# Kernel optimization log

Hardware: AMD Instinct MI355X
Metric: run time of the kernel (lower is better)

## Reference

```python
import jax, jax.numpy as jnp
import numpy as np

N, B, D = 2048, 4, 2048   # seq_len, batch, embed_dim (sequence-first layout)
E = 2                     # expand_ratio
H = D // E                # number of heads
EPS = 1e-5


def setup_inputs() -> dict:
    key = jax.random.key(0)
    ks = jax.random.split(key, 3)
    x = jax.random.normal(ks[0], (N, B, D), dtype=jnp.float32)
    W_in = jax.random.normal(ks[1], (3 * D, D), dtype=jnp.float32) / np.sqrt(D).astype(np.float32)
    b_in = jnp.zeros((3 * D,), jnp.float32)
    W_out = jax.random.normal(ks[2], (D, D), dtype=jnp.float32) / np.sqrt(D).astype(np.float32)
    b_out = jnp.zeros((D,), jnp.float32)
    gamma = jnp.ones((D,), jnp.float32)
    beta = jnp.zeros((D,), jnp.float32)
    return {"x": x, "W_in": W_in, "b_in": b_in, "gamma": gamma, "beta": beta,
            "W_out": W_out, "b_out": b_out}


def _linear_scan(lam, u):
    # h_t = lam_t * h_{t-1} + u_t along time axis 0 (HgruRealFunction)
    def combine(c1, c2):
        a1, b1 = c1
        a2, b2 = c2
        return a1 * a2, a2 * b1 + b2
    _, h = jax.lax.associative_scan(combine, (lam, u), axis=0)
    return h


def _layernorm(x, gamma, beta):
    mu = jnp.mean(x, axis=-1, keepdims=True)
    var = jnp.var(x, axis=-1, keepdims=True)
    return (x - mu) * jax.lax.rsqrt(var + EPS) * gamma + beta


def reference(x, W_in, b_in, gamma, beta, W_out, b_out):
    n, b, d = x.shape
    feat = x @ W_in.T + b_in                       # (n,b,3d)
    inp, og, fg = jnp.split(feat, 3, axis=-1)
    inp = jax.nn.silu(inp)                         # act_fun = silu
    og = jax.nn.sigmoid(og)                        # uv_act_fun = sigmoid
    lam = jax.nn.sigmoid(fg)                       # lower_bound = 0 => lambda = sigmoid(F)

    inp = inp.reshape(n, b, H, E)
    og = og.reshape(n, b, H, E)
    lam = lam.reshape(n, b, H, E)

    # input = einsum('...hd,...he->...hde', 1-lambda, input)
    u = ((1.0 - lam)[..., :, None] * inp[..., None, :]).reshape(n, b, H * E * E)
    lam_f = jnp.broadcast_to(lam[..., :, None], (n, b, H, E, E)).reshape(n, b, H * E * E)

    s_fwd = _linear_scan(lam_f, u)
    s_rev = jnp.flip(_linear_scan(jnp.flip(lam_f, 0), jnp.flip(u, 0)), 0)
    s = (s_fwd + s_rev).reshape(n, b, H, E, E)

    o = jnp.einsum('nbhde,nbhd->nbhe', s, og).reshape(n, b, d)
    o = _layernorm(o, gamma, beta)
    return o @ W_out.T + b_out
```

## Files before the change

### kernel.cpp

```cpp
#include <hip/hip_runtime.h>
#include <hip/hip_bf16.h>

#define NSEQ 2048
#define NB   4
#define DIM  2048
#define HN   1024
#define FC   6144
#define MROWS 8192
#define CHUNKS 64
#define CLEN 32
#define NCH  4096

typedef __bf16 bf16x8_t __attribute__((ext_vector_type(8)));
typedef float  f32x4_t  __attribute__((ext_vector_type(4)));

__device__ __forceinline__ float sigm(float x){ return 1.f/(1.f + __expf(-x)); }
__device__ __forceinline__ float bflo(unsigned p){ return __uint_as_float(p << 16); }
__device__ __forceinline__ float bfhi(unsigned p){ return __uint_as_float(p & 0xffff0000u); }
__device__ __forceinline__ unsigned short f2bf(float f){
  union { __hip_bfloat16 h; unsigned short u; } cv;
  cv.h = __float2bfloat16(f);
  return cv.u;
}

__global__ __launch_bounds__(256) void cvt_bf16_4(const float4* __restrict__ in,
                                                  ushort4* __restrict__ out, int n4){
  int i = blockIdx.x * blockDim.x + threadIdx.x;
  int st = gridDim.x * blockDim.x;
  for (; i < n4; i += st){
    float4 v = in[i];
    ushort4 r;
    r.x = f2bf(v.x); r.y = f2bf(v.y); r.z = f2bf(v.z); r.w = f2bf(v.w);
    out[i] = r;
  }
}

__device__ __forceinline__ void gl_lds16(const void* g, void* l){
  __builtin_amdgcn_global_load_lds((const __attribute__((address_space(1))) void*)g,
                                   (__attribute__((address_space(3))) void*)l, 16, 0, 0);
}

template <typename OutT>
__global__ __launch_bounds__(512, 2) void gemm256(const __hip_bfloat16* __restrict__ A,
                                                  const __hip_bfloat16* __restrict__ B,
                                                  const float* __restrict__ bias,
                                                  OutT* __restrict__ C,
                                                  int M, int N, int K, int nbx){
  __shared__ __align__(16) __hip_bfloat16 smem[3*16384];
  const int tid  = threadIdx.x;
  const int wave = tid >> 6, lane = tid & 63;

  const int cpx = gridDim.x >> 3;
  const int wg  = (blockIdx.x & 7) * cpx + (blockIdx.x >> 3);
  const int bx = wg % nbx, by = wg / nbx;
  const int m0 = by * 256, n0 = bx * 256;

  const int wr = wave >> 2, wc = wave & 3;
  const int r  = lane & 15, q = lane >> 4;
  const int kph = (q ^ (r & 3)) * 8;

  auto stage = [&](int kt, int bo){
    #pragma unroll
    for (int i = 0; i < 2; ++i){
      int g = i*512 + tid;
      int row = g >> 2;
      int k16 = (g & 3) ^ (row & 3);
      gl_lds16(A + (size_t)(m0 + row)*K + kt + k16*8, smem + bo + g*8);
      gl_lds16(B + (size_t)(n0 + row)*K + kt + k16*8, smem + bo + 8192 + g*8);
    }
  };
  const int arow = (wr*128 + r) * 32 + kph;
  const int brow = 8192 + (wc*64 + r) * 32 + kph;

  f32x4_t acc[8][4] = {};
  const int NT = K >> 5;

  stage(0, 0);
  stage(32, 16384);
  __syncthreads();

  bf16x8_t Fa[8], Fb[4];
  #pragma unroll
  for (int i = 0; i < 8; ++i) Fa[i] = *reinterpret_cast<const bf16x8_t*>(smem + arow + i*512);
  #pragma unroll
  for (int j = 0; j < 4; ++j) Fb[j] = *reinterpret_cast<const bf16x8_t*>(smem + brow + j*512);

  for (int t = 0; t < NT; ++t){
    int b2 = 16384 * ((t+2) % 3);
    if (t + 2 < NT) stage((t+2)*32, b2);
    int rb = (t+1 < NT) ? 16384*((t+1)%3) : 16384*(t%3);
    bf16x8_t Na[8], Nb[4];
    #pragma unroll
    for (int j = 0; j < 4; ++j) Nb[j] = *reinterpret_cast<const bf16x8_t*>(smem + rb + brow + j*512);
    #pragma unroll
    for (int i = 0; i < 8; ++i) Na[i] = *reinterpret_cast<const bf16x8_t*>(smem + rb + arow + i*512);
    __builtin_amdgcn_s_setprio(1);
    #pragma unroll
    for (int i = 0; i < 8; ++i)
      #pragma unroll
      for (int j = 0; j < 4; ++j)
        acc[i][j] = __builtin_amdgcn_mfma_f32_16x16x32_bf16(Fa[i], Fb[j], acc[i][j], 0, 0, 0);
    __builtin_amdgcn_s_setprio(0);
    __syncthreads();
    #pragma unroll
    for (int i = 0; i < 8; ++i) Fa[i] = Na[i];
    #pragma unroll
    for (int j = 0; j < 4; ++j) Fb[j] = Nb[j];
  }

  #pragma unroll
  for (int fn = 0; fn < 4; ++fn){
    int col = n0 + wc*64 + fn*16 + r;
    float bv = bias[col];
    #pragma unroll
    for (int fm = 0; fm < 8; ++fm){
      int row0 = m0 + wr*128 + fm*16 + q*4;
      #pragma unroll
      for (int j = 0; j < 4; ++j){
        float v = acc[fm][fn][j] + bv;
        if constexpr (__is_same(OutT, float))
          C[(size_t)(row0 + j)*N + col] = v;
        else
          C[(size_t)(row0 + j)*N + col] = __float2bfloat16(v);
      }
    }
  }
}

struct SV { float l0, l1, u00, u01, u10, u11; };
__device__ __forceinline__ SV stepv(const unsigned* __restrict__ fp, int rowu){
  unsigned pi = fp[rowu];
  unsigned pf = fp[rowu + 2048];
  SV s;
  s.l0 = sigm(bflo(pf)); s.l1 = sigm(bfhi(pf));
  float i0 = bflo(pi), i1 = bfhi(pi);
  i0 *= sigm(i0); i1 *= sigm(i1);
  float a0 = 1.f - s.l0, a1 = 1.f - s.l1;
  s.u00 = a0*i0; s.u01 = a0*i1; s.u10 = a1*i0; s.u11 = a1*i1;
  return s;
}

__global__ __launch_bounds__(256) void scan_agg(const unsigned* __restrict__ feat,
    float* __restrict__ aggP, float4* __restrict__ aggHF, float4* __restrict__ aggHR){
  int ch = blockIdx.x*256 + threadIdx.x;
  int c  = blockIdx.y;
  int b = ch >> 10, h = ch & 1023;
  int base = b*3072 + h;
  int n0 = c*CLEN;
  float P0 = 1.f, P1 = 1.f;
  float f00=0,f01=0,f10=0,f11=0;
  for (int t = 0; t < CLEN; ++t){
    SV s = stepv(feat, (n0+t)*12288 + base);
    f00 = s.l0*f00 + s.u00; f01 = s.l0*f01 + s.u01;
    f10 = s.l1*f10 + s.u10; f11 = s.l1*f11 + s.u11;
    P0 *= s.l0; P1 *= s.l1;
  }
  float r00=0,r01=0,r10=0,r11=0;
  for (int t = CLEN-1; t >= 0; --t){
    SV s = stepv(feat, (n0+t)*12288 + base);
    r00 = s.l0*r00 + s.u00; r01 = s.l0*r01 + s.u01;
    r10 = s.l1*r10 + s.u10; r11 = s.l1*r11 + s.u11;
  }
  aggP[c*8192 + ch*2]     = P0;
  aggP[c*8192 + ch*2 + 1] = P1;
  aggHF[c*4096 + ch] = make_float4(f00,f01,f10,f11);
  aggHR[c*4096 + ch] = make_float4(r00,r01,r10,r11);
}

__global__ __launch_bounds__(256) void scan_carry(const float* __restrict__ aggP,
    const float* __restrict__ aggHF, const float* __restrict__ aggHR,
    float* __restrict__ cF, float* __restrict__ cR){
  int t  = blockIdx.x*256 + threadIdx.x;
  int pd = t >> 1;
  float s = 0.f;
  for (int c = 0; c < CHUNKS; ++c){
    cF[c*16384 + t] = s;
    s = aggP[c*8192 + pd]*s + aggHF[c*16384 + t];
  }
  s = 0.f;
  for (int c = CHUNKS-1; c >= 0; --c){
    cR[c*16384 + t] = s;
    s = aggP[c*8192 + pd]*s + aggHR[c*16384 + t];
  }
}

__global__ __launch_bounds__(256) void scan_fr(const unsigned* __restrict__ feat,
    const float4* __restrict__ cF, const float4* __restrict__ cR,
    float2* __restrict__ o){
  int ch = blockIdx.x*256 + threadIdx.x;
  int c  = blockIdx.y;
  int b = ch >> 10, h = ch & 1023;
  int base = b*3072 + h;
  float2 accv[CLEN];
  {
    float4 hv = cF[c*4096 + ch];
    float h00=hv.x, h01=hv.y, h10=hv.z, h11=hv.w;
    #pragma unroll
    for (int t = 0; t < CLEN; ++t){
      int rowu = (c*CLEN + t)*12288 + base;
      SV s = stepv(feat, rowu);
      h00 = s.l0*h00 + s.u00; h01 = s.l0*h01 + s.u01;
      h10 = s.l1*h10 + s.u10; h11 = s.l1*h11 + s.u11;
      unsigned po = feat[rowu + 1024];
      float g0 = sigm(bflo(po)), g1 = sigm(bfhi(po));
      accv[t] = make_float2(g0*h00 + g1*h10, g0*h01 + g1*h11);
    }
  }
  {
    float4 hv = cR[c*4096 + ch];
    float h00=hv.x, h01=hv.y, h10=hv.z, h11=hv.w;
    #pragma unroll
    for (int t = CLEN-1; t >= 0; --t){
      int rowu = (c*CLEN + t)*12288 + base;
      SV s = stepv(feat, rowu);
      h00 = s.l0*h00 + s.u00; h01 = s.l0*h01 + s.u01;
      h10 = s.l1*h10 + s.u10; h11 = s.l1*h11 + s.u11;
      unsigned po = feat[rowu + 1024];
      float g0 = sigm(bflo(po)), g1 = sigm(bfhi(po));
      accv[t].x += g0*h00 + g1*h10;
      accv[t].y += g0*h01 + g1*h11;
    }
  }
  #pragma unroll
  for (int t = 0; t < CLEN; ++t)
    o[((c*CLEN + t)*NB + b)*1024 + h] = accv[t];
}

__global__ __launch_bounds__(256) void layernorm_k(const float* __restrict__ o,
    const float* __restrict__ gamma, const float* __restrict__ beta,
    __hip_bfloat16* __restrict__ out){
  int row = blockIdx.x, t = threadIdx.x;
  const float4* x = (const float4*)(o + (size_t)row*DIM);
  float4 a = x[t], b = x[t + 256];
  float s  = (a.x + a.y) + (a.z + a.w) + (b.x + b.y) + (b.z + b.w);
  float ss = (a.x*a.x + a.y*a.y) + (a.z*a.z + a.w*a.w)
           + (b.x*b.x + b.y*b.y) + (b.z*b.z + b.w*b.w);
  #pragma unroll
  for (int off = 32; off > 0; off >>= 1){
    s  += __shfl_down(s, off);
    ss += __shfl_down(ss, off);
  }
  __shared__ float red[8];
  int wv = t >> 6, ln = t & 63;
  if (ln == 0){ red[wv] = s; red[4 + wv] = ss; }
  __syncthreads();
  float S  = (red[0] + red[1]) + (red[2] + red[3]);
  float SS = (red[4] + red[5]) + (red[6] + red[7]);
  float mu = S * (1.f/DIM);
  float rs = rsqrtf(SS * (1.f/DIM) - mu*mu + 1e-5f);
  const float4* gp = (const float4*)gamma;
  const float4* bp = (const float4*)beta;
  float4 g0 = gp[t], g1 = gp[t + 256], be0 = bp[t], be1 = bp[t + 256];
  ushort4* op = (ushort4*)(out + (size_t)row*DIM);
  ushort4 r0, r1;
  r0.x = f2bf((a.x - mu)*rs*g0.x + be0.x);
  r0.y = f2bf((a.y - mu)*rs*g0.y + be0.y);
  r0.z = f2bf((a.z - mu)*rs*g0.z + be0.z);
  r0.w = f2bf((a.w - mu)*rs*g0.w + be0.w);
  r1.x = f2bf((b.x - mu)*rs*g1.x + be1.x);
  r1.y = f2bf((b.y - mu)*rs*g1.y + be1.y);
  r1.z = f2bf((b.z - mu)*rs*g1.z + be1.z);
  r1.w = f2bf((b.w - mu)*rs*g1.w + be1.w);
  op[t] = r0; op[t + 256] = r1;
}

extern "C" void kernel_launch(void* const* d_in, const int* in_sizes, int n_in,
                              void* d_out, int out_size, void* d_ws, size_t ws_size,
                              hipStream_t stream){
  (void)in_sizes; (void)n_in; (void)out_size;
  const float* x     = (const float*)d_in[0];
  const float* W_in  = (const float*)d_in[1];
  const float* b_in  = (const float*)d_in[2];
  const float* gamma = (const float*)d_in[3];
  const float* beta  = (const float*)d_in[4];
  const float* W_out = (const float*)d_in[5];
  const float* b_out = (const float*)d_in[6];
  float* out = (float*)d_out;

  char* p = (char*)d_ws;
  auto carve = [&](size_t bytes) -> char* {
    char* r = p; p += (bytes + 255) & ~(size_t)255; return r;
  };
  __hip_bfloat16* feat = (__hip_bfloat16*)carve((size_t)MROWS*FC*2);
  char* U              = carve((size_t)MROWS*DIM*4);
  __hip_bfloat16* Wob  = (__hip_bfloat16*)carve((size_t)DIM*DIM*2);
  float* aggP  = (float*)carve((size_t)CHUNKS*8192*4);
  float* aggHF = (float*)carve((size_t)CHUNKS*16384*4);
  float* aggHR = (float*)carve((size_t)CHUNKS*16384*4);
  float* cF    = (float*)carve((size_t)CHUNKS*16384*4);
  float* cR    = (float*)carve((size_t)CHUNKS*16384*4);
  if ((size_t)(p - (char*)d_ws) > ws_size) return;

  __hip_bfloat16* xb  = (__hip_bfloat16*)U;
  __hip_bfloat16* Wib = (__hip_bfloat16*)(U + (size_t)MROWS*DIM*2);
  float* o            = (float*)U;
  __hip_bfloat16* oln = (__hip_bfloat16*)feat;

  cvt_bf16_4<<<2048, 256, 0, stream>>>((const float4*)x,     (ushort4*)xb,  MROWS*DIM/4);
  cvt_bf16_4<<<2048, 256, 0, stream>>>((const float4*)W_in,  (ushort4*)Wib, FC*DIM/4);
  cvt_bf16_4<<<1024, 256, 0, stream>>>((const float4*)W_out, (ushort4*)Wob, DIM*DIM/4);

  gemm256<__hip_bfloat16><<<768, 512, 0, stream>>>(xb, Wib, b_in, feat, MROWS, FC, 2048, FC/256);

  scan_agg  <<<dim3(NCH/256, CHUNKS), 256, 0, stream>>>((const unsigned*)feat, aggP, (float4*)aggHF, (float4*)aggHR);
  scan_carry<<<64, 256, 0, stream>>>(aggP, aggHF, aggHR, cF, cR);
  scan_fr   <<<dim3(NCH/256, CHUNKS), 256, 0, stream>>>((const unsigned*)feat, (const float4*)cF, (const float4*)cR, (float2*)o);

  layernorm_k<<<MROWS, 256, 0, stream>>>(o, gamma, beta, oln);

  gemm256<float><<<256, 512, 0, stream>>>(oln, Wob, b_out, out, MROWS, DIM, 2048, DIM/256);
}
```

Measured before the change: 496.5 us.

## Restructure GEMM main loop into 8-phase ping-pong pipeline with half-tile staging

Rewrites the bf16 GEMM main loop to use a K tile of 64 split into half-tiles across two LDS slots (128KB of LDS). Each of eight phases loads fragments, issues one half-tile global-to-LDS load, then synchronizes with explicit vmcnt/lgkmcnt waits and raw barriers before a block of MFMAs. It also switches to a new XOR swizzle layout with two rows packed per 64-element line. The aim is finer-grained overlap of memory and MFMA work with fewer full syncthreads. In exchange, the LDS use doubles, which with launch_bounds(512,2) may limit occupancy, and the hand-tuned waitcnt counts are fragile.

```diff
diff --git a/kernel.cpp b/kernel.cpp
--- a/kernel.cpp
+++ b/kernel.cpp
@@ -40,13 +40,42 @@
                                    (__attribute__((address_space(3))) void*)l, 16, 0, 0);
 }
 
+template<int SLOT,int KSUB,int MH,bool VM, class SG>
+__device__ __forceinline__ void do_phase(const __hip_bfloat16* smem,
+    const int* aoff, const int* boff, bf16x8_t (&Bf)[4], f32x4_t (&acc)[8][4], SG&& sg){
+  if (VM) asm volatile("s_waitcnt vmcnt(6)" ::: "memory");
+  const __hip_bfloat16* base = smem + SLOT*32768 + KSUB*8192;
+  bf16x8_t Af[4];
+  #pragma unroll
+  for (int mi = 0; mi < 4; ++mi)
+    Af[mi] = *reinterpret_cast<const bf16x8_t*>(base + aoff[MH*4 + mi]);
+  if (MH == 0){
+    #pragma unroll
+    for (int n = 0; n < 4; ++n)
+      Bf[n] = *reinterpret_cast<const bf16x8_t*>(base + 16384 + boff[n]);
+  }
+  sg();
+  __builtin_amdgcn_s_barrier();
+  asm volatile("s_waitcnt lgkmcnt(0)" ::: "memory");
+  __builtin_amdgcn_sched_barrier(0);
+  __builtin_amdgcn_s_setprio(1);
+  #pragma unroll
+  for (int mi = 0; mi < 4; ++mi)
+    #pragma unroll
+    for (int n = 0; n < 4; ++n)
+      acc[MH*4 + mi][n] =
+        __builtin_amdgcn_mfma_f32_16x16x32_bf16(Af[mi], Bf[n], acc[MH*4 + mi][n], 0, 0, 0);
+  __builtin_amdgcn_s_setprio(0);
+  __builtin_amdgcn_s_barrier();
+}
+
 template <typename OutT>
 __global__ __launch_bounds__(512, 2) void gemm256(const __hip_bfloat16* __restrict__ A,
                                                   const __hip_bfloat16* __restrict__ B,
                                                   const float* __restrict__ bias,
                                                   OutT* __restrict__ C,
                                                   int M, int N, int K, int nbx){
-  __shared__ __align__(16) __hip_bfloat16 smem[3*16384];
+  __shared__ __align__(16) __hip_bfloat16 smem[65536];
   const int tid  = threadIdx.x;
   const int wave = tid >> 6, lane = tid & 63;
 
@@ -57,55 +86,55 @@
 
   const int wr = wave >> 2, wc = wave & 3;
   const int r  = lane & 15, q = lane >> 4;
-  const int kph = (q ^ (r & 3)) * 8;
-
-  auto stage = [&](int kt, int bo){
+  const int NT = K >> 6;
+
+  int aoff[8], boff[4];
+  #pragma unroll
+  for (int f = 0; f < 8; ++f){
+    int R = wr*128 + (f>>2)*64 + (f&3)*16 + r;
+    aoff[f] = (R>>1)*64 + (((((R&1)<<2) | q) ^ ((R>>1)&7)) << 3);
+  }
+  #pragma unroll
+  for (int n = 0; n < 4; ++n){
+    int R = wc*64 + n*16 + r;
+    boff[n] = (R>>1)*64 + (((((R&1)<<2) | q) ^ ((R>>1)&7)) << 3);
+  }
+
+  auto stage_half = [&](int slot, int ab, int khalf, int ktile){
+    if (ktile >= NT) return;
+    const __hip_bfloat16* Base = ab ? B : A;
+    const int t0 = ab ? n0 : m0;
+    const int kc = ktile*64 + khalf*32;
+    const int hb = slot*32768 + ab*16384 + khalf*8192;
     #pragma unroll
     for (int i = 0; i < 2; ++i){
       int g = i*512 + tid;
-      int row = g >> 2;
-      int k16 = (g & 3) ^ (row & 3);
-      gl_lds16(A + (size_t)(m0 + row)*K + kt + k16*8, smem + bo + g*8);
-      gl_lds16(B + (size_t)(n0 + row)*K + kt + k16*8, smem + bo + 8192 + g*8);
+      int line = g >> 3, glp = g & 7;
+      int glog = glp ^ (line & 7);
+      int row = line*2 + (glog >> 2);
+      int kg = glog & 3;
+      gl_lds16(Base + (size_t)(t0 + row)*K + kc + kg*8, smem + hb + g*8);
     }
   };
-  const int arow = (wr*128 + r) * 32 + kph;
-  const int brow = 8192 + (wc*64 + r) * 32 + kph;
 
   f32x4_t acc[8][4] = {};
-  const int NT = K >> 5;
-
-  stage(0, 0);
-  stage(32, 16384);
-  __syncthreads();
-
-  bf16x8_t Fa[8], Fb[4];
-  #pragma unroll
-  for (int i = 0; i < 8; ++i) Fa[i] = *reinterpret_cast<const bf16x8_t*>(smem + arow + i*512);
-  #pragma unroll
-  for (int j = 0; j < 4; ++j) Fb[j] = *reinterpret_cast<const bf16x8_t*>(smem + brow + j*512);
-
-  for (int t = 0; t < NT; ++t){
-    int b2 = 16384 * ((t+2) % 3);
-    if (t + 2 < NT) stage((t+2)*32, b2);
-    int rb = (t+1 < NT) ? 16384*((t+1)%3) : 16384*(t%3);
-    bf16x8_t Na[8], Nb[4];
-    #pragma unroll
-    for (int j = 0; j < 4; ++j) Nb[j] = *reinterpret_cast<const bf16x8_t*>(smem + rb + brow + j*512);
-    #pragma unroll
-    for (int i = 0; i < 8; ++i) Na[i] = *reinterpret_cast<const bf16x8_t*>(smem + rb + arow + i*512);
-    __builtin_amdgcn_s_setprio(1);
-    #pragma unroll
-    for (int i = 0; i < 8; ++i)
-      #pragma unroll
-      for (int j = 0; j < 4; ++j)
-        acc[i][j] = __builtin_amdgcn_mfma_f32_16x16x32_bf16(Fa[i], Fb[j], acc[i][j], 0, 0, 0);
-    __builtin_amdgcn_s_setprio(0);
-    __syncthreads();
-    #pragma unroll
-    for (int i = 0; i < 8; ++i) Fa[i] = Na[i];
-    #pragma unroll
-    for (int j = 0; j < 4; ++j) Fb[j] = Nb[j];
+  bf16x8_t Bf[4];
+
+  stage_half(0,0,0, 0); stage_half(0,1,0, 0); stage_half(0,0,1, 0); stage_half(0,1,1, 0);
+  stage_half(1,1,0, 1); stage_half(1,0,0, 1); stage_half(1,1,1, 1);
+  asm volatile("s_waitcnt vmcnt(6)" ::: "memory");
+  __builtin_amdgcn_s_barrier();
+
+  for (int j = 0; j < NT/2; ++j){
+    const int kb = 2*j;
+    do_phase<0,0,0,true >(smem, aoff, boff, Bf, acc, [&]{ stage_half(1,0,1, kb+1); });
+    do_phase<0,0,1,false>(smem, aoff, boff, Bf, acc, [&]{ stage_half(0,1,0, kb+2); });
+    do_phase<0,1,0,true >(smem, aoff, boff, Bf, acc, [&]{ stage_half(0,0,0, kb+2); });
+    do_phase<0,1,1,false>(smem, aoff, boff, Bf, acc, [&]{ stage_half(0,1,1, kb+2); });
+    do_phase<1,0,0,true >(smem, aoff, boff, Bf, acc, [&]{ stage_half(0,0,1, kb+2); });
+    do_phase<1,0,1,false>(smem, aoff, boff, Bf, acc, [&]{ stage_half(1,1,0, kb+3); });
+    do_phase<1,1,0,true >(smem, aoff, boff, Bf, acc, [&]{ stage_half(1,0,0, kb+3); });
+    do_phase<1,1,1,false>(smem, aoff, boff, Bf, acc, [&]{ stage_half(1,1,1, kb+3); });
   }
 
   #pragma unroll
@@ -116,12 +145,12 @@
     for (int fm = 0; fm < 8; ++fm){
       int row0 = m0 + wr*128 + fm*16 + q*4;
       #pragma unroll
-      for (int j = 0; j < 4; ++j){
-        float v = acc[fm][fn][j] + bv;
+      for (int jj = 0; jj < 4; ++jj){
+        float v = acc[fm][fn][jj] + bv;
         if constexpr (__is_same(OutT, float))
-          C[(size_t)(row0 + j)*N + col] = v;
+          C[(size_t)(row0 + jj)*N + col] = v;
         else
-          C[(size_t)(row0 + j)*N + col] = __float2bfloat16(v);
+          C[(size_t)(row0 + jj)*N + col] = __float2bfloat16(v);
       }
     }
   }
```

Measured after the change: 479.8 us. 3.4% less time.

## Switch GEMMs to 256x128 tiles with double buffering; cache scan inputs in registers

Applied to the files above, without the earlier changes.

Both GEMMs now use a 256x128 block tile with 256 threads (4 waves) instead of 256x256 with 512 threads. The LDS pipeline drops from triple to double buffering and gets a new XOR swizzle over row pairs. Register prefetch of the next fragments is replaced by loading fragments at the start of each iteration. The chunk-aggregate scan keeps its 32 loaded feature words per channel in registers, so the reverse pass does not reload them from global memory. Risks: less load/compute overlap in the GEMM, twice as many blocks, and higher register pressure in the scan kernel.

```diff
diff --git a/kernel.cpp b/kernel.cpp
--- a/kernel.cpp
+++ b/kernel.cpp
@@ -41,71 +41,79 @@
 }
 
 template <typename OutT>
-__global__ __launch_bounds__(512, 2) void gemm256(const __hip_bfloat16* __restrict__ A,
-                                                  const __hip_bfloat16* __restrict__ B,
-                                                  const float* __restrict__ bias,
-                                                  OutT* __restrict__ C,
-                                                  int M, int N, int K, int nbx){
-  __shared__ __align__(16) __hip_bfloat16 smem[3*16384];
+__global__ __launch_bounds__(256, 2) void gemm256x128(const __hip_bfloat16* __restrict__ A,
+                                                      const __hip_bfloat16* __restrict__ B,
+                                                      const float* __restrict__ bias,
+                                                      OutT* __restrict__ C,
+                                                      int M, int N, int K, int nbx){
+  __shared__ __align__(16) __hip_bfloat16 smem[2*12288];
   const int tid  = threadIdx.x;
   const int wave = tid >> 6, lane = tid & 63;
 
   const int cpx = gridDim.x >> 3;
   const int wg  = (blockIdx.x & 7) * cpx + (blockIdx.x >> 3);
   const int bx = wg % nbx, by = wg / nbx;
-  const int m0 = by * 256, n0 = bx * 256;
-
-  const int wr = wave >> 2, wc = wave & 3;
+  const int m0 = by * 256, n0 = bx * 128;
+
+  const int wr = wave >> 1, wc = wave & 1;
   const int r  = lane & 15, q = lane >> 4;
-  const int kph = (q ^ (r & 3)) * 8;
+  const int NT = K >> 5;
+
+  int aoff[8], boff[4];
+  #pragma unroll
+  for (int f = 0; f < 8; ++f){
+    int R = wr*128 + f*16 + r;
+    aoff[f] = (R>>1)*64 + (((((R&1)<<2) | q) ^ ((R>>1)&7)) << 3);
+  }
+  #pragma unroll
+  for (int n = 0; n < 4; ++n){
+    int R = wc*64 + n*16 + r;
+    boff[n] = (R>>1)*64 + (((((R&1)<<2) | q) ^ ((R>>1)&7)) << 3);
+  }
 
   auto stage = [&](int kt, int bo){
     #pragma unroll
+    for (int i = 0; i < 4; ++i){
+      int g = i*256 + tid;
+      int line = g >> 3, glog = (g & 7) ^ (line & 7);
+      int row = line*2 + (glog >> 2), kg = glog & 3;
+      gl_lds16(A + (size_t)(m0 + row)*K + kt + kg*8, smem + bo + g*8);
+    }
+    #pragma unroll
     for (int i = 0; i < 2; ++i){
-      int g = i*512 + tid;
-      int row = g >> 2;
-      int k16 = (g & 3) ^ (row & 3);
-      gl_lds16(A + (size_t)(m0 + row)*K + kt + k16*8, smem + bo + g*8);
-      gl_lds16(B + (size_t)(n0 + row)*K + kt + k16*8, smem + bo + 8192 + g*8);
+      int g = i*256 + tid;
+      int line = g >> 3, glog = (g & 7) ^ (line & 7);
+      int row = line*2 + (glog >> 2), kg = glog & 3;
+      gl_lds16(B + (size_t)(n0 + row)*K + kt + kg*8, smem + bo + 8192 + g*8);
     }
   };
-  const int arow = (wr*128 + r) * 32 + kph;
-  const int brow = 8192 + (wc*64 + r) * 32 + kph;
 
   f32x4_t acc[8][4] = {};
-  const int NT = K >> 5;
 
   stage(0, 0);
-  stage(32, 16384);
   __syncthreads();
-
-  bf16x8_t Fa[8], Fb[4];
-  #pragma unroll
-  for (int i = 0; i < 8; ++i) Fa[i] = *reinterpret_cast<const bf16x8_t*>(smem + arow + i*512);
-  #pragma unroll
-  for (int j = 0; j < 4; ++j) Fb[j] = *reinterpret_cast<const bf16x8_t*>(smem + brow + j*512);
+  int buf = 0;
 
   for (int t = 0; t < NT; ++t){
-    int b2 = 16384 * ((t+2) % 3);
-    if (t + 2 < NT) stage((t+2)*32, b2);
-    int rb = (t+1 < NT) ? 16384*((t+1)%3) : 16384*(t%3);
-    bf16x8_t Na[8], Nb[4];
-    #pragma unroll
-    for (int j = 0; j < 4; ++j) Nb[j] = *reinterpret_cast<const bf16x8_t*>(smem + rb + brow + j*512);
-    #pragma unroll
-    for (int i = 0; i < 8; ++i) Na[i] = *reinterpret_cast<const bf16x8_t*>(smem + rb + arow + i*512);
+    if (t + 1 < NT) stage((t+1)*32, (buf^1)*12288);
+    const __hip_bfloat16* Ab = smem + buf*12288;
+    const __hip_bfloat16* Bb = Ab + 8192;
+    bf16x8_t bfr[4], af[8];
+    #pragma unroll
+    for (int fn = 0; fn < 4; ++fn)
+      bfr[fn] = *reinterpret_cast<const bf16x8_t*>(Bb + boff[fn]);
+    #pragma unroll
+    for (int fm = 0; fm < 8; ++fm)
+      af[fm] = *reinterpret_cast<const bf16x8_t*>(Ab + aoff[fm]);
     __builtin_amdgcn_s_setprio(1);
     #pragma unroll
-    for (int i = 0; i < 8; ++i)
+    for (int fm = 0; fm < 8; ++fm)
       #pragma unroll
-      for (int j = 0; j < 4; ++j)
-        acc[i][j] = __builtin_amdgcn_mfma_f32_16x16x32_bf16(Fa[i], Fb[j], acc[i][j], 0, 0, 0);
+      for (int fn = 0; fn < 4; ++fn)
+        acc[fm][fn] = __builtin_amdgcn_mfma_f32_16x16x32_bf16(af[fm], bfr[fn], acc[fm][fn], 0, 0, 0);
     __builtin_amdgcn_s_setprio(0);
     __syncthreads();
-    #pragma unroll
-    for (int i = 0; i < 8; ++i) Fa[i] = Na[i];
-    #pragma unroll
-    for (int j = 0; j < 4; ++j) Fb[j] = Nb[j];
+    buf ^= 1;
   }
 
   #pragma unroll
@@ -128,9 +136,7 @@
 }
 
 struct SV { float l0, l1, u00, u01, u10, u11; };
-__device__ __forceinline__ SV stepv(const unsigned* __restrict__ fp, int rowu){
-  unsigned pi = fp[rowu];
-  unsigned pf = fp[rowu + 2048];
+__device__ __forceinline__ SV stepp(unsigned pi, unsigned pf){
   SV s;
   s.l0 = sigm(bflo(pf)); s.l1 = sigm(bfhi(pf));
   float i0 = bflo(pi), i1 = bfhi(pi);
@@ -139,6 +145,9 @@
   s.u00 = a0*i0; s.u01 = a0*i1; s.u10 = a1*i0; s.u11 = a1*i1;
   return s;
 }
+__device__ __forceinline__ SV stepv(const unsigned* __restrict__ fp, int rowu){
+  return stepp(fp[rowu], fp[rowu + 2048]);
+}
 
 __global__ __launch_bounds__(256) void scan_agg(const unsigned* __restrict__ feat,
     float* __restrict__ aggP, float4* __restrict__ aggHF, float4* __restrict__ aggHR){
@@ -147,17 +156,23 @@
   int b = ch >> 10, h = ch & 1023;
   int base = b*3072 + h;
   int n0 = c*CLEN;
+  unsigned spi[CLEN], spf[CLEN];
   float P0 = 1.f, P1 = 1.f;
   float f00=0,f01=0,f10=0,f11=0;
+  #pragma unroll
   for (int t = 0; t < CLEN; ++t){
-    SV s = stepv(feat, (n0+t)*12288 + base);
+    int rowu = (n0+t)*12288 + base;
+    spi[t] = feat[rowu];
+    spf[t] = feat[rowu + 2048];
+    SV s = stepp(spi[t], spf[t]);
     f00 = s.l0*f00 + s.u00; f01 = s.l0*f01 + s.u01;
     f10 = s.l1*f10 + s.u10; f11 = s.l1*f11 + s.u11;
     P0 *= s.l0; P1 *= s.l1;
   }
   float r00=0,r01=0,r10=0,r11=0;
+  #pragma unroll
   for (int t = CLEN-1; t >= 0; --t){
-    SV s = stepv(feat, (n0+t)*12288 + base);
+    SV s = stepp(spi[t], spf[t]);
     r00 = s.l0*r00 + s.u00; r01 = s.l0*r01 + s.u01;
     r10 = s.l1*r10 + s.u10; r11 = s.l1*r11 + s.u11;
   }
@@ -300,7 +315,7 @@
   cvt_bf16_4<<<2048, 256, 0, stream>>>((const float4*)W_in,  (ushort4*)Wib, FC*DIM/4);
   cvt_bf16_4<<<1024, 256, 0, stream>>>((const float4*)W_out, (ushort4*)Wob, DIM*DIM/4);
 
-  gemm256<__hip_bfloat16><<<768, 512, 0, stream>>>(xb, Wib, b_in, feat, MROWS, FC, 2048, FC/256);
+  gemm256x128<__hip_bfloat16><<<1536, 256, 0, stream>>>(xb, Wib, b_in, feat, MROWS, FC, 2048, FC/128);
 
   scan_agg  <<<dim3(NCH/256, CHUNKS), 256, 0, stream>>>((const unsigned*)feat, aggP, (float4*)aggHF, (float4*)aggHR);
   scan_carry<<<64, 256, 0, stream>>>(aggP, aggHF, aggHR, cF, cR);
@@ -308,5 +323,5 @@
 
   layernorm_k<<<MROWS, 256, 0, stream>>>(o, gamma, beta, oln);
 
-  gemm256<float><<<256, 512, 0, stream>>>(oln, Wob, b_out, out, MROWS, DIM, 2048, DIM/256);
-}
+  gemm256x128<float><<<512, 256, 0, stream>>>(oln, Wob, b_out, out, MROWS, DIM, 2048, DIM/128);
+}
```

Result: faster. 466.2 us (-6.1%).
